# Kernel optimization log

Measured on AMD Instinct MI355X. Metric: run time of the kernel, lower is better.

The kernel has to match this reference:

```python
import jax, jax.numpy as jnp
import numpy as np

B, CIN, COUT = 2, 64, 64
D, H, W = 8, 32, 32
KD = KH = KW = 3
K = KD * KH * KW  # 27
STRIDE, PAD, DIL = 1, 1, 1
DOUT = (D + 2 * PAD - DIL * (KD - 1) - 1) // STRIDE + 1
HOUT = (H + 2 * PAD - DIL * (KH - 1) - 1) // STRIDE + 1
WOUT = (W + 2 * PAD - DIL * (KW - 1) - 1) // STRIDE + 1


def setup_inputs() -> dict:
    key = jax.random.key(0)
    k1, k2, k3, k4 = jax.random.split(key, 4)
    x = jax.random.normal(k1, (B, CIN, D, H, W), dtype=jnp.float32)
    offset = jax.random.normal(k2, (B, 3 * K, DOUT, HOUT, WOUT), dtype=jnp.float32)
    weight = jax.random.normal(k3, (COUT, CIN, KD, KH, KW), dtype=jnp.float32) * 0.05
    bias = jax.random.normal(k4, (COUT,), dtype=jnp.float32) * 0.1
    return {"x": x, "offset": offset, "weight": weight, "bias": bias}


def _trilinear_sample(xb, zd, zh, zw):
    # xb: [C, D, H, W]; zd/zh/zw: [K, P] float sampling coords (zero padding outside)
    Dd, Hh, Ww = xb.shape[1], xb.shape[2], xb.shape[3]
    d0 = jnp.floor(zd); h0 = jnp.floor(zh); w0 = jnp.floor(zw)
    fd = zd - d0; fh = zh - h0; fw = zw - w0
    d0i = d0.astype(jnp.int32); h0i = h0.astype(jnp.int32); w0i = w0.astype(jnp.int32)
    acc = jnp.zeros((xb.shape[0],) + zd.shape, dtype=xb.dtype)
    for dd in (0, 1):
        for dh in (0, 1):
            for dw in (0, 1):
                di = d0i + dd; hi = h0i + dh; wi = w0i + dw
                wgt = ((fd if dd else 1.0 - fd) * (fh if dh else 1.0 - fh)
                       * (fw if dw else 1.0 - fw))
                valid = ((di >= 0) & (di < Dd) & (hi >= 0) & (hi < Hh)
                         & (wi >= 0) & (wi < Ww)).astype(xb.dtype)
                v = xb[:, jnp.clip(di, 0, Dd - 1), jnp.clip(hi, 0, Hh - 1),
                       jnp.clip(wi, 0, Ww - 1)]  # [C, K, P]
                acc = acc + v * (wgt * valid)[None]
    return acc


def _deform_conv3d(x, offset, weight, bias):
    Bb = x.shape[0]
    P = DOUT * HOUT * WOUT
    # kernel taps
    kd, kh, kw = jnp.unravel_index(jnp.arange(K), (KD, KH, KW))
    # output grid
    od, oh, ow = jnp.meshgrid(jnp.arange(DOUT), jnp.arange(HOUT), jnp.arange(WOUT), indexing="ij")
    base_d = (od[None] * STRIDE - PAD + kd[:, None, None, None] * DIL).astype(jnp.float32)  # [K,Do,Ho,Wo]
    base_h = (oh[None] * STRIDE - PAD + kh[:, None, None, None] * DIL).astype(jnp.float32)
    base_w = (ow[None] * STRIDE - PAD + kw[:, None, None, None] * DIL).astype(jnp.float32)
    off = offset.reshape(Bb, K, 3, DOUT, HOUT, WOUT)  # per-tap (dd, dh, dw)
    zd = (base_d[None] + off[:, :, 0]).reshape(Bb, K, P)
    zh = (base_h[None] + off[:, :, 1]).reshape(Bb, K, P)
    zw = (base_w[None] + off[:, :, 2]).reshape(Bb, K, P)
    sampled = jax.vmap(_trilinear_sample)(x, zd, zh, zw)  # [B, C, K, P]
    wmat = weight.reshape(COUT, CIN, K)
    out = jnp.einsum("bckp,ock->bop", sampled, wmat)  # [B, COUT, P]
    out = out + bias[None, :, None]
    return out.reshape(Bb, COUT, DOUT, HOUT, WOUT)


def reference(x, offset, weight, bias):
    return _deform_conv3d(x, offset, weight, bias)
```

## Files before the change

kernel.cpp:

```cpp
#include <hip/hip_runtime.h>
#include <hip/hip_fp16.h>


#define BB    2
#define CINC  64
#define COUTC 64
#define DDEP  8
#define HGT   32
#define WID   32
#define KK    27
#define KGRP  3
#define KPG   9
#define KPH   3
#define PP    8192
#define TP    64
#define LDW   72

typedef _Float16 f16x8 __attribute__((ext_vector_type(8)));
typedef float f32x4 __attribute__((ext_vector_type(4)));
typedef unsigned int u32x4 __attribute__((ext_vector_type(4)));

__device__ __forceinline__ __half2 h2(unsigned v) { return __builtin_bit_cast(__half2, v); }
__device__ __forceinline__ unsigned h2u(__half2 h) { return __builtin_bit_cast(unsigned, h); }

__device__ __forceinline__ void acc8h(const char* __restrict__ xc, unsigned off, __half2 uu,
                                      __half2& s0, __half2& s1, __half2& s2, __half2& s3) {
    u32x4 v = *(const u32x4*)(xc + off);
    s0 = __hfma2(h2(v.x), uu, s0);
    s1 = __hfma2(h2(v.y), uu, s1);
    s2 = __hfma2(h2(v.z), uu, s2);
    s3 = __hfma2(h2(v.w), uu, s3);
}

#define WBLOCKS 432
#define ZBLOCKS 1024
__global__ void pre_kernel(const float* __restrict__ x, const float* __restrict__ w,
                           unsigned short* __restrict__ xt, unsigned short* __restrict__ wt,
                           float* __restrict__ out) {
    __shared__ float sT[64][65];
    const int t    = threadIdx.x;
    const int lane = t & 63;
    const int wv   = t >> 6;
    const int half = lane >> 5;
    const int c2   = lane & 31;
    int blk = blockIdx.x;
    if (blk < 256) {
        int b  = blk >> 7;
        int s0 = (blk & 127) * 64;
        #pragma unroll
        for (int i = 0; i < 16; ++i) {
            int c = wv * 16 + i;
            sT[c][lane] = x[(size_t)(b * CINC + c) * PP + s0 + lane];
        }
        __syncthreads();
        #pragma unroll
        for (int i = 0; i < 8; ++i) {
            int s = wv * 16 + 2 * i + half;
            unsigned pk = h2u(__floats2half2_rn(sT[2 * c2][s], sT[2 * c2 + 1][s]));
            *(unsigned*)&xt[(size_t)(b * PP + s0 + s) * 64 + 2 * c2] = pk;
        }
    } else if (blk < 256 + WBLOCKS) {
        int id = (blk - 256) * 256 + t;
        if (id < KK * COUTC * CINC) {
            int c = id & 63;
            int o = (id >> 6) & 63;
            int k = id >> 12;
            __half hw = __float2half(w[(o * CINC + c) * KK + k]);
            wt[id] = __builtin_bit_cast(unsigned short, hw);
        }
    } else {
        int id = (blk - 256 - WBLOCKS) * 256 + t;
        ((float4*)out)[id] = make_float4(0.f, 0.f, 0.f, 0.f);
    }
}

__global__ __launch_bounds__(256, 3) void deform_kernel(
    const unsigned short* __restrict__ xt, const float* __restrict__ off,
    const unsigned short* __restrict__ wt, const float* __restrict__ bias,
    float* __restrict__ out)
{
    __shared__ unsigned short sW[KPH * COUTC * LDW] __attribute__((aligned(16)));
    __shared__ unsigned short sS[TP * LDW]          __attribute__((aligned(16)));
    __shared__ int      sIdx[KPH][TP][8] __attribute__((aligned(16)));
    __shared__ unsigned sCfh[KPH][TP][8] __attribute__((aligned(16)));

    const int t     = threadIdx.x;
    const int lane  = t & 63;
    const int wv    = t >> 6;
    const int choct = lane & 7;
    const int g8    = lane >> 3;
    const int ch16  = 16 * choct;
    const int b     = blockIdx.x >> 7;
    const int p0    = (blockIdx.x & 127) * TP;
    const int kg    = blockIdx.y;

    const char* __restrict__ xc = (const char*)xt + (size_t)b * PP * 128;

    f32x4 acc[4];
    #pragma unroll
    for (int g = 0; g < 4; ++g) acc[g] = (f32x4)0.0f;

    const int n0  = lane & 15;
    const int q   = lane >> 4;
    const int cr  = lane & 15;
    const int ckl = lane >> 4;

    #pragma unroll 1
    for (int ph = 0; ph < 3; ++ph) {
        const int kbase = kg * KPG + ph * KPH;

        __syncthreads();

        const unsigned short* wk = wt + kbase * (COUTC * CINC);
        #pragma unroll
        for (int j = 0; j < 6; ++j) {
            int idx = j * 2048 + t * 8;
            int kl  = idx >> 12;
            int rem = idx & 4095;
            *(f16x8*)&sW[kl * (COUTC * LDW) + (rem >> 6) * LDW + (rem & 63)] =
                *(const f16x8*)(wk + idx);
        }

        if (ckl < KPH) {
            int k  = kbase + ckl;
            int pl = 16 * wv + cr;
            int pp = p0 + pl;
            int ow = pp & 31;
            int oh = (pp >> 5) & 31;
            int od = pp >> 10;
            int kd = k / 9;
            int kh = (k - kd * 9) / 3;
            int kw = k - kd * 9 - kh * 3;
            const float* ob = off + (size_t)(b * (3 * KK) + 3 * k) * PP + pp;
            float zd = (float)(od - 1 + kd) + ob[0];
            float zh = (float)(oh - 1 + kh) + ob[PP];
            float zw = (float)(ow - 1 + kw) + ob[2 * PP];

            float fdf = floorf(zd); int d0 = (int)fdf; float fd = zd - fdf;
            float fhf = floorf(zh); int h0 = (int)fhf; float fh = zh - fhf;
            float fwf = floorf(zw); int w0 = (int)fwf; float fw = zw - fwf;

            float Bd0 = (d0 >= 0     && d0 < DDEP)     ? 1.0f - fd : 0.0f;
            float Bd1 = (d0 + 1 >= 0 && d0 + 1 < DDEP) ? fd        : 0.0f;
            float Ch0 = (h0 >= 0     && h0 < HGT)      ? 1.0f - fh : 0.0f;
            float Ch1 = (h0 + 1 >= 0 && h0 + 1 < HGT)  ? fh        : 0.0f;
            float Aw0 = (w0 >= 0     && w0 < WID)      ? 1.0f - fw : 0.0f;
            float Aw1 = (w0 + 1 >= 0 && w0 + 1 < WID)  ? fw        : 0.0f;
            int dc0 = min(max(d0, 0), DDEP - 1);
            int dc1 = min(max(d0 + 1, 0), DDEP - 1);
            int hc0 = min(max(h0, 0), HGT - 1);
            int hc1 = min(max(h0 + 1, 0), HGT - 1);
            int wc0 = min(max(w0, 0), WID - 1);
            int wc1 = min(max(w0 + 1, 0), WID - 1);

            int dhb0 = (dc0 * HGT + hc0) * (WID * 128);
            int dhb1 = (dc0 * HGT + hc1) * (WID * 128);
            int dhb2 = (dc1 * HGT + hc0) * (WID * 128);
            int dhb3 = (dc1 * HGT + hc1) * (WID * 128);
            int wo0 = wc0 * 128, wo1 = wc1 * 128;
            sIdx[ckl][pl][0] = dhb0 + wo0;
            sIdx[ckl][pl][1] = dhb1 + wo0;
            sIdx[ckl][pl][2] = dhb2 + wo0;
            sIdx[ckl][pl][3] = dhb3 + wo0;
            sIdx[ckl][pl][4] = dhb0 + wo1;
            sIdx[ckl][pl][5] = dhb1 + wo1;
            sIdx[ckl][pl][6] = dhb2 + wo1;
            sIdx[ckl][pl][7] = dhb3 + wo1;
            float bc0 = Bd0 * Ch0, bc1 = Bd0 * Ch1, bc2 = Bd1 * Ch0, bc3 = Bd1 * Ch1;
            float u0 = bc0 * Aw0, u1 = bc1 * Aw0, u2 = bc2 * Aw0, u3 = bc3 * Aw0;
            float u4 = bc0 * Aw1, u5 = bc1 * Aw1, u6 = bc2 * Aw1, u7 = bc3 * Aw1;
            sCfh[ckl][pl][0] = h2u(__half2half2(__float2half(u0)));
            sCfh[ckl][pl][1] = h2u(__half2half2(__float2half(u1)));
            sCfh[ckl][pl][2] = h2u(__half2half2(__float2half(u2)));
            sCfh[ckl][pl][3] = h2u(__half2half2(__float2half(u3)));
            sCfh[ckl][pl][4] = h2u(__half2half2(__float2half(u4)));
            sCfh[ckl][pl][5] = h2u(__half2half2(__float2half(u5)));
            sCfh[ckl][pl][6] = h2u(__half2half2(__float2half(u6)));
            sCfh[ckl][pl][7] = h2u(__half2half2(__float2half(u7)));
        }
        __syncthreads();

        #pragma unroll
        for (int kl = 0; kl < KPH; ++kl) {
            #pragma unroll
            for (int it = 0; it < 2; ++it) {
                int prow = 16 * wv + 8 * it + g8;
                const int4 i0 = *(const int4*)&sIdx[kl][prow][0];
                const int4 i1 = *(const int4*)&sIdx[kl][prow][4];
                const u32x4 c0 = *(const u32x4*)&sCfh[kl][prow][0];
                const u32x4 c1 = *(const u32x4*)&sCfh[kl][prow][4];
                __half2 s0 = h2(0u), s1 = h2(0u), s2 = h2(0u), s3 = h2(0u);
                acc8h(xc, (unsigned)(i0.x + ch16), h2(c0.x), s0, s1, s2, s3);
                acc8h(xc, (unsigned)(i0.y + ch16), h2(c0.y), s0, s1, s2, s3);
                acc8h(xc, (unsigned)(i0.z + ch16), h2(c0.z), s0, s1, s2, s3);
                acc8h(xc, (unsigned)(i0.w + ch16), h2(c0.w), s0, s1, s2, s3);
                acc8h(xc, (unsigned)(i1.x + ch16), h2(c1.x), s0, s1, s2, s3);
                acc8h(xc, (unsigned)(i1.y + ch16), h2(c1.y), s0, s1, s2, s3);
                acc8h(xc, (unsigned)(i1.z + ch16), h2(c1.z), s0, s1, s2, s3);
                acc8h(xc, (unsigned)(i1.w + ch16), h2(c1.w), s0, s1, s2, s3);
                u32x4 pk = {h2u(s0), h2u(s1), h2u(s2), h2u(s3)};
                *(u32x4*)&sS[prow * LDW + 8 * choct] = pk;
            }

            {
                const unsigned short* sWk = &sW[kl * (COUTC * LDW)];
                f16x8 b0 = *(const f16x8*)&sS[(16 * wv + n0) * LDW +      8 * q];
                f16x8 b1 = *(const f16x8*)&sS[(16 * wv + n0) * LDW + 32 + 8 * q];
                __builtin_amdgcn_s_setprio(1);
                #pragma unroll
                for (int g = 0; g < 4; ++g) {
                    f16x8 a0 = *(const f16x8*)&sWk[(16 * g + n0) * LDW +      8 * q];
                    f16x8 a1 = *(const f16x8*)&sWk[(16 * g + n0) * LDW + 32 + 8 * q];
                    acc[g] = __builtin_amdgcn_mfma_f32_16x16x32_f16(a0, b0, acc[g], 0, 0, 0);
                    acc[g] = __builtin_amdgcn_mfma_f32_16x16x32_f16(a1, b1, acc[g], 0, 0, 0);
                }
                __builtin_amdgcn_s_setprio(0);
            }
        }
    }

    const int p = p0 + 16 * wv + n0;
    #pragma unroll
    for (int g = 0; g < 4; ++g) {
        #pragma unroll
        for (int r = 0; r < 4; ++r) {
            int o = 16 * g + 4 * q + r;
            float v = acc[g][r];
            if (kg == 0) v += bias[o];
            unsafeAtomicAdd(&out[(size_t)(b * COUTC + o) * PP + p], v);
        }
    }
}

extern "C" void kernel_launch(void* const* d_in, const int* in_sizes, int n_in,
                              void* d_out, int out_size, void* d_ws, size_t ws_size,
                              hipStream_t stream) {
    const float* x    = (const float*)d_in[0];
    const float* off  = (const float*)d_in[1];
    const float* w    = (const float*)d_in[2];
    const float* bias = (const float*)d_in[3];
    float* out        = (float*)d_out;

    unsigned short* xt = (unsigned short*)d_ws;
    unsigned short* wt = (unsigned short*)((char*)d_ws + (size_t)BB * PP * 64 * 2);

    hipLaunchKernelGGL(pre_kernel, dim3(256 + WBLOCKS + ZBLOCKS), dim3(256), 0,
                       stream, x, w, xt, wt, out);
    hipLaunchKernelGGL(deform_kernel, dim3(BB * (PP / TP), KGRP), dim3(256), 0, stream,
                       xt, off, wt, bias, out);
}
```

Before: 92.25 us.

## Split taps across 9 groups, swizzle LDS, compress corner offsets

Each block now handles 3 kernel taps instead of 9, with 9 tap-groups in the grid. This removes the inner phase loop and its barriers and triples the number of blocks, at the cost of three times as many atomic adds to the output. LDS padding is replaced by an XOR swizzle to avoid bank conflicts with smaller buffers. Per-point corner data is packed into a base offset plus three deltas and four paired half2 weights, which halves the coordinate table. Launch bounds are raised to 4 blocks per SM.

```diff
diff --git a/kernel.cpp b/kernel.cpp
--- a/kernel.cpp
+++ b/kernel.cpp
@@ -9,12 +9,10 @@
 #define HGT   32
 #define WID   32
 #define KK    27
-#define KGRP  3
-#define KPG   9
-#define KPH   3
+#define KGRP  9
+#define KPB   3
 #define PP    8192
 #define TP    64
-#define LDW   72
 
 typedef _Float16 f16x8 __attribute__((ext_vector_type(8)));
 typedef float f32x4 __attribute__((ext_vector_type(4)));
@@ -22,8 +20,10 @@
 
 __device__ __forceinline__ __half2 h2(unsigned v) { return __builtin_bit_cast(__half2, v); }
 __device__ __forceinline__ unsigned h2u(__half2 h) { return __builtin_bit_cast(unsigned, h); }
-
-__device__ __forceinline__ void acc8h(const char* __restrict__ xc, unsigned off, __half2 uu,
+__device__ __forceinline__ __half2 blo(unsigned v) { return __half2half2(__low2half(h2(v))); }
+__device__ __forceinline__ __half2 bhi(unsigned v) { return __half2half2(__high2half(h2(v))); }
+
+__device__ __forceinline__ void acc8h(const char* __restrict__ xc, int off, __half2 uu,
                                       __half2& s0, __half2& s1, __half2& s2, __half2& s3) {
     u32x4 v = *(const u32x4*)(xc + off);
     s0 = __hfma2(h2(v.x), uu, s0);
@@ -74,15 +74,14 @@
     }
 }
 
-__global__ __launch_bounds__(256, 3) void deform_kernel(
+__global__ __launch_bounds__(256, 4) void deform_kernel(
     const unsigned short* __restrict__ xt, const float* __restrict__ off,
     const unsigned short* __restrict__ wt, const float* __restrict__ bias,
     float* __restrict__ out)
 {
-    __shared__ unsigned short sW[KPH * COUTC * LDW] __attribute__((aligned(16)));
-    __shared__ unsigned short sS[TP * LDW]          __attribute__((aligned(16)));
-    __shared__ int      sIdx[KPH][TP][8] __attribute__((aligned(16)));
-    __shared__ unsigned sCfh[KPH][TP][8] __attribute__((aligned(16)));
+    __shared__ unsigned short sW[KPB * COUTC * 64] __attribute__((aligned(16)));
+    __shared__ unsigned short sS[TP * 64]          __attribute__((aligned(16)));
+    __shared__ int sCrd[KPB][TP][8] __attribute__((aligned(16)));
 
     const int t     = threadIdx.x;
     const int lane  = t & 63;
@@ -93,8 +92,11 @@
     const int b     = blockIdx.x >> 7;
     const int p0    = (blockIdx.x & 127) * TP;
     const int kg    = blockIdx.y;
+    const int kbase = kg * KPB;
 
     const char* __restrict__ xc = (const char*)xt + (size_t)b * PP * 128;
+    char* sWb = (char*)sW;
+    char* sSb = (char*)sS;
 
     f32x4 acc[4];
     #pragma unroll
@@ -105,117 +107,112 @@
     const int cr  = lane & 15;
     const int ckl = lane >> 4;
 
-    #pragma unroll 1
-    for (int ph = 0; ph < 3; ++ph) {
-        const int kbase = kg * KPG + ph * KPH;
-
-        __syncthreads();
-
+    {
         const unsigned short* wk = wt + kbase * (COUTC * CINC);
         #pragma unroll
         for (int j = 0; j < 6; ++j) {
             int idx = j * 2048 + t * 8;
             int kl  = idx >> 12;
-            int rem = idx & 4095;
-            *(f16x8*)&sW[kl * (COUTC * LDW) + (rem >> 6) * LDW + (rem & 63)] =
+            int o   = (idx >> 6) & 63;
+            int cb  = (idx & 63) * 2;
+            *(f16x8*)(sWb + kl * 8192 + o * 128 + (cb ^ ((o & 7) << 4))) =
                 *(const f16x8*)(wk + idx);
         }
-
-        if (ckl < KPH) {
-            int k  = kbase + ckl;
-            int pl = 16 * wv + cr;
-            int pp = p0 + pl;
-            int ow = pp & 31;
-            int oh = (pp >> 5) & 31;
-            int od = pp >> 10;
-            int kd = k / 9;
-            int kh = (k - kd * 9) / 3;
-            int kw = k - kd * 9 - kh * 3;
-            const float* ob = off + (size_t)(b * (3 * KK) + 3 * k) * PP + pp;
-            float zd = (float)(od - 1 + kd) + ob[0];
-            float zh = (float)(oh - 1 + kh) + ob[PP];
-            float zw = (float)(ow - 1 + kw) + ob[2 * PP];
-
-            float fdf = floorf(zd); int d0 = (int)fdf; float fd = zd - fdf;
-            float fhf = floorf(zh); int h0 = (int)fhf; float fh = zh - fhf;
-            float fwf = floorf(zw); int w0 = (int)fwf; float fw = zw - fwf;
-
-            float Bd0 = (d0 >= 0     && d0 < DDEP)     ? 1.0f - fd : 0.0f;
-            float Bd1 = (d0 + 1 >= 0 && d0 + 1 < DDEP) ? fd        : 0.0f;
-            float Ch0 = (h0 >= 0     && h0 < HGT)      ? 1.0f - fh : 0.0f;
-            float Ch1 = (h0 + 1 >= 0 && h0 + 1 < HGT)  ? fh        : 0.0f;
-            float Aw0 = (w0 >= 0     && w0 < WID)      ? 1.0f - fw : 0.0f;
-            float Aw1 = (w0 + 1 >= 0 && w0 + 1 < WID)  ? fw        : 0.0f;
-            int dc0 = min(max(d0, 0), DDEP - 1);
-            int dc1 = min(max(d0 + 1, 0), DDEP - 1);
-            int hc0 = min(max(h0, 0), HGT - 1);
-            int hc1 = min(max(h0 + 1, 0), HGT - 1);
-            int wc0 = min(max(w0, 0), WID - 1);
-            int wc1 = min(max(w0 + 1, 0), WID - 1);
-
-            int dhb0 = (dc0 * HGT + hc0) * (WID * 128);
-            int dhb1 = (dc0 * HGT + hc1) * (WID * 128);
-            int dhb2 = (dc1 * HGT + hc0) * (WID * 128);
-            int dhb3 = (dc1 * HGT + hc1) * (WID * 128);
-            int wo0 = wc0 * 128, wo1 = wc1 * 128;
-            sIdx[ckl][pl][0] = dhb0 + wo0;
-            sIdx[ckl][pl][1] = dhb1 + wo0;
-            sIdx[ckl][pl][2] = dhb2 + wo0;
-            sIdx[ckl][pl][3] = dhb3 + wo0;
-            sIdx[ckl][pl][4] = dhb0 + wo1;
-            sIdx[ckl][pl][5] = dhb1 + wo1;
-            sIdx[ckl][pl][6] = dhb2 + wo1;
-            sIdx[ckl][pl][7] = dhb3 + wo1;
-            float bc0 = Bd0 * Ch0, bc1 = Bd0 * Ch1, bc2 = Bd1 * Ch0, bc3 = Bd1 * Ch1;
-            float u0 = bc0 * Aw0, u1 = bc1 * Aw0, u2 = bc2 * Aw0, u3 = bc3 * Aw0;
-            float u4 = bc0 * Aw1, u5 = bc1 * Aw1, u6 = bc2 * Aw1, u7 = bc3 * Aw1;
-            sCfh[ckl][pl][0] = h2u(__half2half2(__float2half(u0)));
-            sCfh[ckl][pl][1] = h2u(__half2half2(__float2half(u1)));
-            sCfh[ckl][pl][2] = h2u(__half2half2(__float2half(u2)));
-            sCfh[ckl][pl][3] = h2u(__half2half2(__float2half(u3)));
-            sCfh[ckl][pl][4] = h2u(__half2half2(__float2half(u4)));
-            sCfh[ckl][pl][5] = h2u(__half2half2(__float2half(u5)));
-            sCfh[ckl][pl][6] = h2u(__half2half2(__float2half(u6)));
-            sCfh[ckl][pl][7] = h2u(__half2half2(__float2half(u7)));
-        }
-        __syncthreads();
-
-        #pragma unroll
-        for (int kl = 0; kl < KPH; ++kl) {
+    }
+
+    if (ckl < KPB) {
+        int k  = kbase + ckl;
+        int pl = 16 * wv + cr;
+        int pp = p0 + pl;
+        int ow = pp & 31;
+        int oh = (pp >> 5) & 31;
+        int od = pp >> 10;
+        int kd = k / 9;
+        int kh = (k - kd * 9) / 3;
+        int kw = k - kd * 9 - kh * 3;
+        const float* ob = off + (size_t)(b * (3 * KK) + 3 * k) * PP + pp;
+        float zd = (float)(od - 1 + kd) + ob[0];
+        float zh = (float)(oh - 1 + kh) + ob[PP];
+        float zw = (float)(ow - 1 + kw) + ob[2 * PP];
+
+        float fdf = floorf(zd); int d0 = (int)fdf; float fd = zd - fdf;
+        float fhf = floorf(zh); int h0 = (int)fhf; float fh = zh - fhf;
+        float fwf = floorf(zw); int w0 = (int)fwf; float fw = zw - fwf;
+
+        float Bd0 = (d0 >= 0     && d0 < DDEP)     ? 1.0f - fd : 0.0f;
+        float Bd1 = (d0 + 1 >= 0 && d0 + 1 < DDEP) ? fd        : 0.0f;
+        float Ch0 = (h0 >= 0     && h0 < HGT)      ? 1.0f - fh : 0.0f;
+        float Ch1 = (h0 + 1 >= 0 && h0 + 1 < HGT)  ? fh        : 0.0f;
+        float Aw0 = (w0 >= 0     && w0 < WID)      ? 1.0f - fw : 0.0f;
+        float Aw1 = (w0 + 1 >= 0 && w0 + 1 < WID)  ? fw        : 0.0f;
+        int dc0 = min(max(d0, 0), DDEP - 1);
+        int dc1 = min(max(d0 + 1, 0), DDEP - 1);
+        int hc0 = min(max(h0, 0), HGT - 1);
+        int hc1 = min(max(h0 + 1, 0), HGT - 1);
+        int wc0 = min(max(w0, 0), WID - 1);
+        int wc1 = min(max(w0 + 1, 0), WID - 1);
+
+        int base = (dc0 * HGT + hc0) * (WID * 128) + wc0 * 128;
+        int wD   = (wc1 - wc0) * 128;
+        int hD   = (hc1 - hc0) * (WID * 128);
+        int dD   = (dc1 - dc0) * (HGT * WID * 128);
+        sCrd[ckl][pl][0] = base;
+        sCrd[ckl][pl][1] = wD;
+        sCrd[ckl][pl][2] = hD;
+        sCrd[ckl][pl][3] = dD;
+        float bc0 = Bd0 * Ch0, bc1 = Bd0 * Ch1, bc2 = Bd1 * Ch0, bc3 = Bd1 * Ch1;
+        sCrd[ckl][pl][4] = (int)h2u(__floats2half2_rn(bc0 * Aw0, bc0 * Aw1));
+        sCrd[ckl][pl][5] = (int)h2u(__floats2half2_rn(bc1 * Aw0, bc1 * Aw1));
+        sCrd[ckl][pl][6] = (int)h2u(__floats2half2_rn(bc2 * Aw0, bc2 * Aw1));
+        sCrd[ckl][pl][7] = (int)h2u(__floats2half2_rn(bc3 * Aw0, bc3 * Aw1));
+    }
+    __syncthreads();
+
+    const int sw   = (n0 & 7) << 4;
+    const int cb0  = (16 * q) ^ sw;
+    const int cb1  = (64 + 16 * q) ^ sw;
+    #pragma unroll
+    for (int kl = 0; kl < KPB; ++kl) {
+        #pragma unroll
+        for (int it = 0; it < 2; ++it) {
+            int prow = 16 * wv + 8 * it + g8;
+            const int4  ib = *(const int4*)&sCrd[kl][prow][0];
+            const u32x4 cw = *(const u32x4*)&sCrd[kl][prow][4];
+            int o0 = ib.x + ch16;
+            int o1 = o0 + ib.y;
+            int o2 = o0 + ib.z;
+            int o3 = o2 + ib.y;
+            int o4 = o0 + ib.w;
+            int o5 = o4 + ib.y;
+            int o6 = o4 + ib.z;
+            int o7 = o6 + ib.y;
+            __half2 s0 = h2(0u), s1 = h2(0u), s2 = h2(0u), s3 = h2(0u);
+            acc8h(xc, o0, blo(cw.x), s0, s1, s2, s3);
+            acc8h(xc, o1, bhi(cw.x), s0, s1, s2, s3);
+            acc8h(xc, o2, blo(cw.y), s0, s1, s2, s3);
+            acc8h(xc, o3, bhi(cw.y), s0, s1, s2, s3);
+            acc8h(xc, o4, blo(cw.z), s0, s1, s2, s3);
+            acc8h(xc, o5, bhi(cw.z), s0, s1, s2, s3);
+            acc8h(xc, o6, blo(cw.w), s0, s1, s2, s3);
+            acc8h(xc, o7, bhi(cw.w), s0, s1, s2, s3);
+            u32x4 pk = {h2u(s0), h2u(s1), h2u(s2), h2u(s3)};
+            *(u32x4*)(sSb + prow * 128 + (ch16 ^ ((prow & 7) << 4))) = pk;
+        }
+
+        {
+            const char* sWk = sWb + kl * 8192;
+            const int rowB = (16 * wv + n0) * 128;
+            f16x8 b0 = *(const f16x8*)(sSb + rowB + cb0);
+            f16x8 b1 = *(const f16x8*)(sSb + rowB + cb1);
+            __builtin_amdgcn_s_setprio(1);
             #pragma unroll
-            for (int it = 0; it < 2; ++it) {
-                int prow = 16 * wv + 8 * it + g8;
-                const int4 i0 = *(const int4*)&sIdx[kl][prow][0];
-                const int4 i1 = *(const int4*)&sIdx[kl][prow][4];
-                const u32x4 c0 = *(const u32x4*)&sCfh[kl][prow][0];
-                const u32x4 c1 = *(const u32x4*)&sCfh[kl][prow][4];
-                __half2 s0 = h2(0u), s1 = h2(0u), s2 = h2(0u), s3 = h2(0u);
-                acc8h(xc, (unsigned)(i0.x + ch16), h2(c0.x), s0, s1, s2, s3);
-                acc8h(xc, (unsigned)(i0.y + ch16), h2(c0.y), s0, s1, s2, s3);
-                acc8h(xc, (unsigned)(i0.z + ch16), h2(c0.z), s0, s1, s2, s3);
-                acc8h(xc, (unsigned)(i0.w + ch16), h2(c0.w), s0, s1, s2, s3);
-                acc8h(xc, (unsigned)(i1.x + ch16), h2(c1.x), s0, s1, s2, s3);
-                acc8h(xc, (unsigned)(i1.y + ch16), h2(c1.y), s0, s1, s2, s3);
-                acc8h(xc, (unsigned)(i1.z + ch16), h2(c1.z), s0, s1, s2, s3);
-                acc8h(xc, (unsigned)(i1.w + ch16), h2(c1.w), s0, s1, s2, s3);
-                u32x4 pk = {h2u(s0), h2u(s1), h2u(s2), h2u(s3)};
-                *(u32x4*)&sS[prow * LDW + 8 * choct] = pk;
+            for (int g = 0; g < 4; ++g) {
+                f16x8 a0 = *(const f16x8*)(sWk + (16 * g + n0) * 128 + cb0);
+                f16x8 a1 = *(const f16x8*)(sWk + (16 * g + n0) * 128 + cb1);
+                acc[g] = __builtin_amdgcn_mfma_f32_16x16x32_f16(a0, b0, acc[g], 0, 0, 0);
+                acc[g] = __builtin_amdgcn_mfma_f32_16x16x32_f16(a1, b1, acc[g], 0, 0, 0);
             }
-
-            {
-                const unsigned short* sWk = &sW[kl * (COUTC * LDW)];
-                f16x8 b0 = *(const f16x8*)&sS[(16 * wv + n0) * LDW +      8 * q];
-                f16x8 b1 = *(const f16x8*)&sS[(16 * wv + n0) * LDW + 32 + 8 * q];
-                __builtin_amdgcn_s_setprio(1);
-                #pragma unroll
-                for (int g = 0; g < 4; ++g) {
-                    f16x8 a0 = *(const f16x8*)&sWk[(16 * g + n0) * LDW +      8 * q];
-                    f16x8 a1 = *(const f16x8*)&sWk[(16 * g + n0) * LDW + 32 + 8 * q];
-                    acc[g] = __builtin_amdgcn_mfma_f32_16x16x32_f16(a0, b0, acc[g], 0, 0, 0);
-                    acc[g] = __builtin_amdgcn_mfma_f32_16x16x32_f16(a1, b1, acc[g], 0, 0, 0);
-                }
-                __builtin_amdgcn_s_setprio(0);
-            }
+            __builtin_amdgcn_s_setprio(0);
         }
     }
 
```

Measured after the change: 101.9 us. 10.5% more time.
